# Performance work log

Hardware: AMD Instinct MI355X
Metric: run time of the kernel (lower is better)

The kernel has to match this reference:

```python
import jax, jax.numpy as jnp
import numpy as np

B, H, W, C = 16, 128, 128, 192
WS, SHIFT, HEADS = 8, 4, 6
N = WS * WS
HD = C // HEADS
SCALE = HD ** -0.5
EPS = 1e-5


def _rel_pos_index():
    coords = np.stack(np.meshgrid(np.arange(WS), np.arange(WS), indexing='ij')).reshape(2, -1)
    rel = (coords[:, :, None] - coords[:, None, :]).transpose(1, 2, 0)
    rel[..., 0] += WS - 1
    rel[..., 1] += WS - 1
    rel[..., 0] *= 2 * WS - 1
    return rel.sum(-1)  # [N, N] int


def _attn_mask():
    img = np.zeros((H, W), np.float32)
    sl = [(0, H - WS), (H - WS, H - SHIFT), (H - SHIFT, H)]
    cnt = 0
    for h0, h1 in sl:
        for w0, w1 in sl:
            img[h0:h1, w0:w1] = cnt
            cnt += 1
    mw = img.reshape(H // WS, WS, W // WS, WS).transpose(0, 2, 1, 3).reshape(-1, N)
    am = mw[:, None, :] - mw[:, :, None]
    return np.where(am != 0, np.float32(-100.0), np.float32(0.0))  # [nW, N, N]


REL_IDX = jnp.asarray(_rel_pos_index())
ATTN_MASK = jnp.asarray(_attn_mask())


def _ln(x, g, b):
    mu = x.mean(-1, keepdims=True)
    var = ((x - mu) ** 2).mean(-1, keepdims=True)
    return (x - mu) * jax.lax.rsqrt(var + EPS) * g + b


def setup_inputs() -> dict:
    key = jax.random.key(0)
    ks = jax.random.split(key, 12)
    d = {
        'x': jax.random.normal(ks[0], (B, H * W, C), jnp.float32),
        'norm1_g': jnp.ones((C,), jnp.float32),
        'norm1_b': jnp.zeros((C,), jnp.float32),
        'qkv_w': jax.random.normal(ks[1], (3 * C, C), jnp.float32) * 0.02,
        'qkv_b': jnp.zeros((3 * C,), jnp.float32),
        'proj_w': jax.random.normal(ks[2], (C, C), jnp.float32) * 0.02,
        'proj_b': jnp.zeros((C,), jnp.float32),
        'rpb_table': jax.random.normal(ks[3], ((2 * WS - 1) ** 2, HEADS), jnp.float32) * 0.02,
        'norm2_g': jnp.ones((C,), jnp.float32),
        'norm2_b': jnp.zeros((C,), jnp.float32),
        'fc1_w': jax.random.normal(ks[4], (4 * C, C), jnp.float32) * 0.02,
        'fc1_b': jnp.zeros((4 * C,), jnp.float32),
        'fc2_w': jax.random.normal(ks[5], (C, 4 * C), jnp.float32) * 0.02,
        'fc2_b': jnp.zeros((C,), jnp.float32),
    }
    return d


def reference(x, norm1_g, norm1_b, qkv_w, qkv_b, proj_w, proj_b, rpb_table,
              norm2_g, norm2_b, fc1_w, fc1_b, fc2_w, fc2_b):
    shortcut = x
    h = _ln(x, norm1_g, norm1_b).reshape(B, H, W, C)
    # cyclic shift (SW-MSA)
    h = jnp.roll(h, shift=(-SHIFT, -SHIFT), axis=(1, 2))
    # window partition -> [B*nW, N, C]
    h = h.reshape(B, H // WS, WS, W // WS, WS, C).transpose(0, 1, 3, 2, 4, 5)
    xw = h.reshape(-1, N, C)
    Bw = xw.shape[0]
    nW = (H // WS) * (W // WS)
    # qkv projection
    qkv = xw @ qkv_w.T + qkv_b  # [Bw, N, 3C]
    qkv = qkv.reshape(Bw, N, 3, HEADS, HD).transpose(2, 0, 3, 1, 4)
    q, k, v = qkv[0], qkv[1], qkv[2]  # [Bw, HEADS, N, HD]
    attn = jnp.einsum('bhnd,bhmd->bhnm', q * SCALE, k)
    # relative position bias gather: [N*N, HEADS] -> [HEADS, N, N]
    bias = rpb_table[REL_IDX.reshape(-1)].reshape(N, N, HEADS).transpose(2, 0, 1)
    attn = attn + bias[None]
    # shift mask add per-window
    attn = attn.reshape(B, nW, HEADS, N, N) + ATTN_MASK[None, :, None, :, :]
    attn = jax.nn.softmax(attn.reshape(Bw, HEADS, N, N), axis=-1)
    out = jnp.einsum('bhnm,bhmd->bhnd', attn, v)
    out = out.transpose(0, 2, 1, 3).reshape(Bw, N, C)
    out = out @ proj_w.T + proj_b
    # window reverse
    out = out.reshape(B, H // WS, W // WS, WS, WS, C).transpose(0, 1, 3, 2, 4, 5)
    out = out.reshape(B, H, W, C)
    out = jnp.roll(out, shift=(SHIFT, SHIFT), axis=(1, 2)).reshape(B, H * W, C)
    h = shortcut + out
    # MLP with residual
    m = _ln(h, norm2_g, norm2_b)
    m = jax.nn.gelu(m @ fc1_w.T + fc1_b, approximate=False)
    m = m @ fc2_w.T + fc2_b
    return h + m
```

## Files before the change

kernel.cpp:

```cpp
#include <hip/hip_runtime.h>
#include <hip/hip_bf16.h>

typedef __bf16 bf16;
typedef __bf16 bf16x8 __attribute__((ext_vector_type(8)));
typedef float f32x4 __attribute__((ext_vector_type(4)));

#define MFMA16(a, b, c) __builtin_amdgcn_mfma_f32_16x16x32_bf16(a, b, c, 0, 0, 0)

#define SCALE_Q 0.17677669529663687f

__global__ __launch_bounds__(256) void prep_kernel(
    const float* __restrict__ qkv_w, const float* __restrict__ proj_w,
    const float* __restrict__ fc1_w, const float* __restrict__ fc2_w,
    const float* __restrict__ rpb,
    bf16* __restrict__ wqkv, bf16* __restrict__ wproj,
    bf16* __restrict__ wfc1, bf16* __restrict__ wfc2,
    float* __restrict__ bias_full) {
  const int i = blockIdx.x * 256 + threadIdx.x;
  if (i < 110592) wqkv[i] = (bf16)qkv_w[i];
  if (i < 36864)  wproj[i] = (bf16)proj_w[i];
  if (i < 147456) { wfc1[i] = (bf16)fc1_w[i]; wfc2[i] = (bf16)fc2_w[i]; }
  if (i < 24576) {
    const int head = i >> 12;
    const int row = (i >> 6) & 63, col = i & 63;
    const int idx = ((row >> 3) - (col >> 3) + 7) * 15 + ((row & 7) - (col & 7) + 7);
    bias_full[i] = rpb[idx * 6 + head];
  }
}

__device__ __forceinline__ int region8(int tok, int wy, int wx) {
  const int gh = wy * 8 + (tok >> 3), gw = wx * 8 + (tok & 7);
  const int rs = (gh < 120) ? 0 : ((gh < 124) ? 1 : 2);
  const int cs = (gw < 120) ? 0 : ((gw < 124) ? 1 : 2);
  return rs * 3 + cs;
}

__global__ __launch_bounds__(384, 3) void swin_block_kernel(
    const float* __restrict__ x,
    const float* __restrict__ n1g, const float* __restrict__ n1b,
    const bf16* __restrict__ wqkv, const float* __restrict__ qkv_b,
    const bf16* __restrict__ wproj, const float* __restrict__ proj_b,
    const float* __restrict__ bias_full,
    const float* __restrict__ n2g, const float* __restrict__ n2b,
    const bf16* __restrict__ wfc1, const float* __restrict__ fc1_b,
    const bf16* __restrict__ wfc2, const float* __restrict__ fc2_b,
    float* __restrict__ out) {
  __shared__ __align__(16) char smem[80896];
  bf16*  a_s  = (bf16*)(smem);
  bf16*  q_s  = (bf16*)(smem);
  bf16*  k_s  = (bf16*)(smem + 24576);
  bf16*  vT_s = (bf16*)(smem + 49152);
  bf16*  ao_s = (bf16*)(smem);
  float* red_s = (float*)(smem + 25600);
  bf16*  m_s  = (bf16*)(smem + 29696);
  bf16*  g_s  = (bf16*)(smem + 55296);

  const int lane = threadIdx.x & 63, waveid = threadIdx.x >> 6;
  const int c = lane & 15, quad = lane >> 4;
  const int window = blockIdx.x;
  const int bi = window >> 8, w_in = window & 255;
  const int wy = w_in >> 4, wx = w_in & 15;
  const f32x4 fzero = {0.f, 0.f, 0.f, 0.f};

  auto p_ptr = [&](int head, int row, int colbyte) -> bf16* {
    int off = (row << 7) + colbyte;
    off ^= (row & 7) << 4;
    return (bf16*)(smem + (head << 13) + off);
  };

  for (int it = 0; it < 11; it++) {
    const int n = waveid * 11 + it;
    if (n < 64) {
      const int oh = (wy * 8 + (n >> 3) + 4) & 127;
      const int ow = (wx * 8 + (n & 7) + 4) & 127;
      const float* xr = x + (size_t)(bi * 16384 + oh * 128 + ow) * 192;
      float v0 = xr[lane], v1 = xr[lane + 64], v2 = xr[lane + 128];
      float s = v0 + v1 + v2;
      float s2 = v0 * v0 + v1 * v1 + v2 * v2;
#pragma unroll
      for (int off = 1; off < 64; off <<= 1) {
        s += __shfl_xor(s, off);
        s2 += __shfl_xor(s2, off);
      }
      const float mu = s * (1.f / 192.f);
      const float rinv = rsqrtf(s2 * (1.f / 192.f) - mu * mu + 1e-5f);
      a_s[n * 200 + lane]       = (bf16)((v0 - mu) * rinv * n1g[lane]       + n1b[lane]);
      a_s[n * 200 + lane + 64]  = (bf16)((v1 - mu) * rinv * n1g[lane + 64]  + n1b[lane + 64]);
      a_s[n * 200 + lane + 128] = (bf16)((v2 - mu) * rinv * n1g[lane + 128] + n1b[lane + 128]);
    }
  }
  __syncthreads();

  {
    f32x4 acc[4][6];
#pragma unroll
    for (int i = 0; i < 4; i++)
#pragma unroll
      for (int j = 0; j < 6; j++) acc[i][j] = fzero;
#pragma unroll
    for (int ks = 0; ks < 6; ks++) {
      bf16x8 a[4], w[6];
#pragma unroll
      for (int i = 0; i < 4; i++)
        a[i] = *(const bf16x8*)&a_s[(16 * i + c) * 200 + ks * 32 + quad * 8];
#pragma unroll
      for (int j = 0; j < 6; j++)
        w[j] = *(const bf16x8*)(wqkv +
            (size_t)(waveid * 96 + 16 * j + c) * 192 + ks * 32 + quad * 8);
#pragma unroll
      for (int i = 0; i < 4; i++)
#pragma unroll
        for (int j = 0; j < 6; j++) acc[i][j] = MFMA16(a[i], w[j], acc[i][j]);
    }
    __syncthreads();
    const int which = waveid >> 1;
#pragma unroll
    for (int j = 0; j < 6; j++) {
      const int col = waveid * 96 + 16 * j + c;
      const int sub = col - which * 192;
      const int head = sub >> 5, d = sub & 31;
      const float bias = qkv_b[col];
#pragma unroll
      for (int i = 0; i < 4; i++)
#pragma unroll
        for (int r = 0; r < 4; r++) {
          const int n = 16 * i + 4 * quad + r;
          const float val = acc[i][j][r] + bias;
          if (which == 0)      q_s[head * 2048 + n * 32 + d] = (bf16)(val * SCALE_Q);
          else if (which == 1) k_s[head * 2048 + n * 32 + d] = (bf16)val;
          else                 vT_s[head * 2048 + d * 64 + n] = (bf16)val;
        }
    }
  }
  __syncthreads();

  f32x4 o[4][2];
  {
    const int head = waveid;
    bf16x8 aq[4], bk[4];
#pragma unroll
    for (int i = 0; i < 4; i++)
      aq[i] = *(const bf16x8*)&q_s[head * 2048 + (16 * i + c) * 32 + quad * 8];
#pragma unroll
    for (int j = 0; j < 4; j++)
      bk[j] = *(const bf16x8*)&k_s[head * 2048 + (16 * j + c) * 32 + quad * 8];
    __syncthreads();

    f32x4 s[4][4];
#pragma unroll
    for (int i = 0; i < 4; i++)
#pragma unroll
      for (int j = 0; j < 4; j++) s[i][j] = fzero;
#pragma unroll
    for (int i = 0; i < 4; i++)
#pragma unroll
      for (int j = 0; j < 4; j++) s[i][j] = MFMA16(aq[i], bk[j], s[i][j]);

    const float* bfp = bias_full + head * 4096;
#pragma unroll
    for (int i = 0; i < 4; i++)
#pragma unroll
      for (int r = 0; r < 4; r++) {
        const int row = 16 * i + 4 * quad + r;
#pragma unroll
        for (int j = 0; j < 4; j++) s[i][j][r] += bfp[row * 64 + 16 * j + c];
      }

    if (wy == 15 || wx == 15) {
      int creg[4];
#pragma unroll
      for (int j = 0; j < 4; j++) creg[j] = region8(16 * j + c, wy, wx);
#pragma unroll
      for (int i = 0; i < 4; i++)
#pragma unroll
        for (int r = 0; r < 4; r++) {
          const int rreg = region8(16 * i + 4 * quad + r, wy, wx);
#pragma unroll
          for (int j = 0; j < 4; j++)
            if (rreg != creg[j]) s[i][j][r] -= 100.f;
        }
    }

#pragma unroll
    for (int i = 0; i < 4; i++)
#pragma unroll
      for (int r = 0; r < 4; r++) {
        float mx = fmaxf(fmaxf(s[i][0][r], s[i][1][r]), fmaxf(s[i][2][r], s[i][3][r]));
#pragma unroll
        for (int off = 1; off < 16; off <<= 1) mx = fmaxf(mx, __shfl_xor(mx, off));
        float sum = 0.f;
#pragma unroll
        for (int j = 0; j < 4; j++) {
          const float p = __expf(s[i][j][r] - mx);
          s[i][j][r] = p;
          sum += p;
        }
#pragma unroll
        for (int off = 1; off < 16; off <<= 1) sum += __shfl_xor(sum, off);
        const float inv = 1.f / sum;
        const int row = 16 * i + 4 * quad + r;
#pragma unroll
        for (int j = 0; j < 4; j++)
          *p_ptr(head, row, (16 * j + c) * 2) = (bf16)(s[i][j][r] * inv);
      }

#pragma unroll
    for (int i = 0; i < 4; i++)
#pragma unroll
      for (int tn = 0; tn < 2; tn++) o[i][tn] = fzero;
#pragma unroll
    for (int ks = 0; ks < 2; ks++) {
      bf16x8 ap[4], bv[2];
#pragma unroll
      for (int i = 0; i < 4; i++)
        ap[i] = *(const bf16x8*)p_ptr(head, 16 * i + c, ks * 64 + quad * 16);
#pragma unroll
      for (int tn = 0; tn < 2; tn++)
        bv[tn] = *(const bf16x8*)&vT_s[head * 2048 + (16 * tn + c) * 64 + ks * 32 + quad * 8];
#pragma unroll
      for (int i = 0; i < 4; i++)
#pragma unroll
        for (int tn = 0; tn < 2; tn++) o[i][tn] = MFMA16(ap[i], bv[tn], o[i][tn]);
    }
  }
  __syncthreads();

#pragma unroll
  for (int i = 0; i < 4; i++)
#pragma unroll
    for (int tn = 0; tn < 2; tn++)
#pragma unroll
      for (int r = 0; r < 4; r++)
        ao_s[(16 * i + 4 * quad + r) * 200 + waveid * 32 + 16 * tn + c] = (bf16)o[i][tn][r];
  __syncthreads();

  float hreg[4][2][4];
  {
    f32x4 acc[4][2];
#pragma unroll
    for (int i = 0; i < 4; i++)
#pragma unroll
      for (int j = 0; j < 2; j++) acc[i][j] = fzero;
#pragma unroll
    for (int ks = 0; ks < 6; ks++) {
      bf16x8 a[4], w[2];
#pragma unroll
      for (int i = 0; i < 4; i++)
        a[i] = *(const bf16x8*)&ao_s[(16 * i + c) * 200 + ks * 32 + quad * 8];
#pragma unroll
      for (int j = 0; j < 2; j++)
        w[j] = *(const bf16x8*)(wproj +
            (size_t)(waveid * 32 + 16 * j + c) * 192 + ks * 32 + quad * 8);
#pragma unroll
      for (int i = 0; i < 4; i++)
#pragma unroll
        for (int j = 0; j < 2; j++) acc[i][j] = MFMA16(a[i], w[j], acc[i][j]);
    }
#pragma unroll
    for (int i = 0; i < 4; i++)
#pragma unroll
      for (int r = 0; r < 4; r++) {
        const int n = 16 * i + 4 * quad + r;
        const int oh = (wy * 8 + (n >> 3) + 4) & 127;
        const int ow = (wx * 8 + (n & 7) + 4) & 127;
        const float* xr = x + (size_t)(bi * 16384 + oh * 128 + ow) * 192;
#pragma unroll
        for (int j = 0; j < 2; j++) {
          const int col = waveid * 32 + 16 * j + c;
          hreg[i][j][r] = acc[i][j][r] + proj_b[col] + xr[col];
        }
      }
  }

#pragma unroll
  for (int i = 0; i < 4; i++)
#pragma unroll
    for (int r = 0; r < 4; r++) {
      float s1 = hreg[i][0][r] + hreg[i][1][r];
      float s2 = hreg[i][0][r] * hreg[i][0][r] + hreg[i][1][r] * hreg[i][1][r];
#pragma unroll
      for (int off = 1; off < 16; off <<= 1) {
        s1 += __shfl_xor(s1, off);
        s2 += __shfl_xor(s2, off);
      }
      if (c == 0) {
        const int n = 16 * i + 4 * quad + r;
        red_s[n * 16 + waveid] = s1;
        red_s[n * 16 + 8 + waveid] = s2;
      }
    }
  __syncthreads();
  {
    const int col0 = waveid * 32 + c, col1 = col0 + 16;
    const float g0 = n2g[col0], b0 = n2b[col0];
    const float g1 = n2g[col1], b1 = n2b[col1];
#pragma unroll
    for (int i = 0; i < 4; i++)
#pragma unroll
      for (int r = 0; r < 4; r++) {
        const int n = 16 * i + 4 * quad + r;
        const f32x4 lo = *(const f32x4*)&red_s[n * 16 + 0];
        const f32x4 hi = *(const f32x4*)&red_s[n * 16 + 4];
        const f32x4 qlo = *(const f32x4*)&red_s[n * 16 + 8];
        const f32x4 qhi = *(const f32x4*)&red_s[n * 16 + 12];
        const float s1 = lo[0] + lo[1] + lo[2] + lo[3] + hi[0] + hi[1];
        const float s2 = qlo[0] + qlo[1] + qlo[2] + qlo[3] + qhi[0] + qhi[1];
        const float mu = s1 * (1.f / 192.f);
        const float rinv = rsqrtf(s2 * (1.f / 192.f) - mu * mu + 1e-5f);
        m_s[n * 200 + col0] = (bf16)((hreg[i][0][r] - mu) * rinv * g0 + b0);
        m_s[n * 200 + col1] = (bf16)((hreg[i][1][r] - mu) * rinv * g1 + b1);
      }
  }
  __syncthreads();

  f32x4 oacc[4][2];
#pragma unroll
  for (int i = 0; i < 4; i++)
#pragma unroll
    for (int j = 0; j < 2; j++) oacc[i][j] = fzero;

  for (int chunk = 0; chunk < 4; chunk++) {
    f32x4 gacc[4][2];
#pragma unroll
    for (int i = 0; i < 4; i++)
#pragma unroll
      for (int j = 0; j < 2; j++) gacc[i][j] = fzero;
#pragma unroll
    for (int ks = 0; ks < 6; ks++) {
      bf16x8 a[4], w[2];
#pragma unroll
      for (int i = 0; i < 4; i++)
        a[i] = *(const bf16x8*)&m_s[(16 * i + c) * 200 + ks * 32 + quad * 8];
#pragma unroll
      for (int j = 0; j < 2; j++)
        w[j] = *(const bf16x8*)(wfc1 +
            (size_t)(chunk * 192 + waveid * 32 + 16 * j + c) * 192 + ks * 32 + quad * 8);
#pragma unroll
      for (int i = 0; i < 4; i++)
#pragma unroll
        for (int j = 0; j < 2; j++) gacc[i][j] = MFMA16(a[i], w[j], gacc[i][j]);
    }
#pragma unroll
    for (int i = 0; i < 4; i++)
#pragma unroll
      for (int j = 0; j < 2; j++) {
        const int lcol = waveid * 32 + 16 * j + c;
        const float fb = fc1_b[chunk * 192 + lcol];
#pragma unroll
        for (int r = 0; r < 4; r++) {
          float val = gacc[i][j][r] + fb;
          val = 0.5f * val * (1.f + erff(val * 0.70710678118654752f));
          g_s[(16 * i + 4 * quad + r) * 200 + lcol] = (bf16)val;
        }
      }
    __syncthreads();
#pragma unroll
    for (int ks = 0; ks < 6; ks++) {
      bf16x8 a[4], w[2];
#pragma unroll
      for (int i = 0; i < 4; i++)
        a[i] = *(const bf16x8*)&g_s[(16 * i + c) * 200 + ks * 32 + quad * 8];
#pragma unroll
      for (int j = 0; j < 2; j++)
        w[j] = *(const bf16x8*)(wfc2 +
            (size_t)(waveid * 32 + 16 * j + c) * 768 + chunk * 192 + ks * 32 + quad * 8);
#pragma unroll
      for (int i = 0; i < 4; i++)
#pragma unroll
        for (int j = 0; j < 2; j++) oacc[i][j] = MFMA16(a[i], w[j], oacc[i][j]);
    }
    __syncthreads();
  }

#pragma unroll
  for (int i = 0; i < 4; i++)
#pragma unroll
    for (int r = 0; r < 4; r++) {
      const int n = 16 * i + 4 * quad + r;
      const int oh = (wy * 8 + (n >> 3) + 4) & 127;
      const int ow = (wx * 8 + (n & 7) + 4) & 127;
      float* orow = out + (size_t)(bi * 16384 + oh * 128 + ow) * 192;
#pragma unroll
      for (int j = 0; j < 2; j++) {
        const int col = waveid * 32 + 16 * j + c;
        orow[col] = oacc[i][j][r] + fc2_b[col] + hreg[i][j][r];
      }
    }
}

extern "C" void kernel_launch(void* const* d_in, const int* in_sizes, int n_in,
                              void* d_out, int out_size, void* d_ws, size_t ws_size,
                              hipStream_t stream) {
  const float* x      = (const float*)d_in[0];
  const float* n1g    = (const float*)d_in[1];
  const float* n1b    = (const float*)d_in[2];
  const float* qkv_w  = (const float*)d_in[3];
  const float* qkv_b  = (const float*)d_in[4];
  const float* proj_w = (const float*)d_in[5];
  const float* proj_b = (const float*)d_in[6];
  const float* rpb    = (const float*)d_in[7];
  const float* n2g    = (const float*)d_in[8];
  const float* n2b    = (const float*)d_in[9];
  const float* fc1_w  = (const float*)d_in[10];
  const float* fc1_b  = (const float*)d_in[11];
  const float* fc2_w  = (const float*)d_in[12];
  const float* fc2_b  = (const float*)d_in[13];

  char* ws = (char*)d_ws;
  float* biasf = (float*)(ws);
  bf16*  wqkv  = (bf16*)(ws + 98304);
  bf16*  wproj = (bf16*)(ws + 98304 + 221184);
  bf16*  wfc1  = (bf16*)(ws + 98304 + 221184 + 73728);
  bf16*  wfc2  = (bf16*)(ws + 98304 + 221184 + 73728 + 294912);

  prep_kernel<<<576, 256, 0, stream>>>(qkv_w, proj_w, fc1_w, fc2_w, rpb,
                                       wqkv, wproj, wfc1, wfc2, biasf);
  swin_block_kernel<<<4096, 384, 0, stream>>>(
      x, n1g, n1b, wqkv, qkv_b, wproj, proj_b, biasf,
      n2g, n2b, wfc1, fc1_b, wfc2, fc2_b, (float*)d_out);
}
```

Baseline: 1.419 ms.

## Spill residual to output buffer, pad V transpose, relax launch bounds

Writes the attention residual h to the output buffer right away and reads it back from global memory in the final epilogue, rather than keeping 32 floats live in registers across the MLP. Stores the transposed V with a padded stride of 72 and packed 4-wide bf16 writes to cut LDS bank conflicts, and reorganises shared memory so the m/g/reduction buffers alias earlier regions. Launch bounds minimum blocks drops from 3 to 1, giving the compiler more registers at the possible cost of occupancy. The extra global round-trip of h adds memory traffic.

Measured after the change: 1.292 ms. 1.1x faster.

```diff
diff --git a/kernel.cpp b/kernel.cpp
--- a/kernel.cpp
+++ b/kernel.cpp
@@ -2,6 +2,7 @@
 #include <hip/hip_bf16.h>
 
 typedef __bf16 bf16;
+typedef __bf16 bf16x4 __attribute__((ext_vector_type(4)));
 typedef __bf16 bf16x8 __attribute__((ext_vector_type(8)));
 typedef float f32x4 __attribute__((ext_vector_type(4)));
 
@@ -35,7 +36,7 @@
   return rs * 3 + cs;
 }
 
-__global__ __launch_bounds__(384, 3) void swin_block_kernel(
+__global__ __launch_bounds__(384, 1) void swin_block_kernel(
     const float* __restrict__ x,
     const float* __restrict__ n1g, const float* __restrict__ n1b,
     const bf16* __restrict__ wqkv, const float* __restrict__ qkv_b,
@@ -45,15 +46,15 @@
     const bf16* __restrict__ wfc1, const float* __restrict__ fc1_b,
     const bf16* __restrict__ wfc2, const float* __restrict__ fc2_b,
     float* __restrict__ out) {
-  __shared__ __align__(16) char smem[80896];
+  __shared__ __align__(16) char smem[76800];
   bf16*  a_s  = (bf16*)(smem);
   bf16*  q_s  = (bf16*)(smem);
   bf16*  k_s  = (bf16*)(smem + 24576);
   bf16*  vT_s = (bf16*)(smem + 49152);
   bf16*  ao_s = (bf16*)(smem);
-  float* red_s = (float*)(smem + 25600);
-  bf16*  m_s  = (bf16*)(smem + 29696);
-  bf16*  g_s  = (bf16*)(smem + 55296);
+  bf16*  m_s  = (bf16*)(smem);
+  bf16*  g_s  = (bf16*)(smem + 25600);
+  float* red_s = (float*)(smem + 51200);
 
   const int lane = threadIdx.x & 63, waveid = threadIdx.x >> 6;
   const int c = lane & 15, quad = lane >> 4;
@@ -114,22 +115,38 @@
     }
     __syncthreads();
     const int which = waveid >> 1;
-#pragma unroll
-    for (int j = 0; j < 6; j++) {
-      const int col = waveid * 96 + 16 * j + c;
-      const int sub = col - which * 192;
-      const int head = sub >> 5, d = sub & 31;
-      const float bias = qkv_b[col];
-#pragma unroll
-      for (int i = 0; i < 4; i++)
-#pragma unroll
-        for (int r = 0; r < 4; r++) {
-          const int n = 16 * i + 4 * quad + r;
-          const float val = acc[i][j][r] + bias;
-          if (which == 0)      q_s[head * 2048 + n * 32 + d] = (bf16)(val * SCALE_Q);
-          else if (which == 1) k_s[head * 2048 + n * 32 + d] = (bf16)val;
-          else                 vT_s[head * 2048 + d * 64 + n] = (bf16)val;
+    if (which == 2) {
+#pragma unroll
+      for (int j = 0; j < 6; j++) {
+        const int col = waveid * 96 + 16 * j + c;
+        const int sub = col - 384;
+        const int head = sub >> 5, d = sub & 31;
+        const float bias = qkv_b[col];
+#pragma unroll
+        for (int i = 0; i < 4; i++) {
+          bf16x4 pk;
+#pragma unroll
+          for (int r = 0; r < 4; r++) pk[r] = (bf16)(acc[i][j][r] + bias);
+          *(bf16x4*)&vT_s[head * 2304 + d * 72 + 16 * i + 4 * quad] = pk;
         }
+      }
+    } else {
+#pragma unroll
+      for (int j = 0; j < 6; j++) {
+        const int col = waveid * 96 + 16 * j + c;
+        const int sub = col - which * 192;
+        const int head = sub >> 5, d = sub & 31;
+        const float bias = qkv_b[col];
+#pragma unroll
+        for (int i = 0; i < 4; i++)
+#pragma unroll
+          for (int r = 0; r < 4; r++) {
+            const int n = 16 * i + 4 * quad + r;
+            const float val = acc[i][j][r] + bias;
+            if (which == 0) q_s[head * 2048 + n * 32 + d] = (bf16)(val * SCALE_Q);
+            else            k_s[head * 2048 + n * 32 + d] = (bf16)val;
+          }
+      }
     }
   }
   __syncthreads();
@@ -216,7 +233,7 @@
         ap[i] = *(const bf16x8*)p_ptr(head, 16 * i + c, ks * 64 + quad * 16);
 #pragma unroll
       for (int tn = 0; tn < 2; tn++)
-        bv[tn] = *(const bf16x8*)&vT_s[head * 2048 + (16 * tn + c) * 64 + ks * 32 + quad * 8];
+        bv[tn] = *(const bf16x8*)&vT_s[head * 2304 + (16 * tn + c) * 72 + ks * 32 + quad * 8];
 #pragma unroll
       for (int i = 0; i < 4; i++)
 #pragma unroll
@@ -234,7 +251,7 @@
         ao_s[(16 * i + 4 * quad + r) * 200 + waveid * 32 + 16 * tn + c] = (bf16)o[i][tn][r];
   __syncthreads();
 
-  float hreg[4][2][4];
+  float hv[4][2][4];
   {
     f32x4 acc[4][2];
 #pragma unroll
@@ -263,11 +280,15 @@
         const int n = 16 * i + 4 * quad + r;
         const int oh = (wy * 8 + (n >> 3) + 4) & 127;
         const int ow = (wx * 8 + (n & 7) + 4) & 127;
-        const float* xr = x + (size_t)(bi * 16384 + oh * 128 + ow) * 192;
+        const size_t base = (size_t)(bi * 16384 + oh * 128 + ow) * 192;
+        const float* xr = x + base;
+        float* orow = out + base;
 #pragma unroll
         for (int j = 0; j < 2; j++) {
           const int col = waveid * 32 + 16 * j + c;
-          hreg[i][j][r] = acc[i][j][r] + proj_b[col] + xr[col];
+          const float h = acc[i][j][r] + proj_b[col] + xr[col];
+          hv[i][j][r] = h;
+          orow[col] = h;
         }
       }
   }
@@ -276,8 +297,8 @@
   for (int i = 0; i < 4; i++)
 #pragma unroll
     for (int r = 0; r < 4; r++) {
-      float s1 = hreg[i][0][r] + hreg[i][1][r];
-      float s2 = hreg[i][0][r] * hreg[i][0][r] + hreg[i][1][r] * hreg[i][1][r];
+      float s1 = hv[i][0][r] + hv[i][1][r];
+      float s2 = hv[i][0][r] * hv[i][0][r] + hv[i][1][r] * hv[i][1][r];
 #pragma unroll
       for (int off = 1; off < 16; off <<= 1) {
         s1 += __shfl_xor(s1, off);
@@ -290,6 +311,7 @@
       }
     }
   __syncthreads();
+
   {
     const int col0 = waveid * 32 + c, col1 = col0 + 16;
     const float g0 = n2g[col0], b0 = n2b[col0];
@@ -307,8 +329,8 @@
         const float s2 = qlo[0] + qlo[1] + qlo[2] + qlo[3] + qhi[0] + qhi[1];
         const float mu = s1 * (1.f / 192.f);
         const float rinv = rsqrtf(s2 * (1.f / 192.f) - mu * mu + 1e-5f);
-        m_s[n * 200 + col0] = (bf16)((hreg[i][0][r] - mu) * rinv * g0 + b0);
-        m_s[n * 200 + col1] = (bf16)((hreg[i][1][r] - mu) * rinv * g1 + b1);
+        m_s[n * 200 + col0] = (bf16)((hv[i][0][r] - mu) * rinv * g0 + b0);
+        m_s[n * 200 + col1] = (bf16)((hv[i][1][r] - mu) * rinv * g1 + b1);
       }
   }
   __syncthreads();
@@ -383,7 +405,8 @@
 #pragma unroll
       for (int j = 0; j < 2; j++) {
         const int col = waveid * 32 + 16 * j + c;
-        orow[col] = oacc[i][j][r] + fc2_b[col] + hreg[i][j][r];
+        const float h = orow[col];
+        orow[col] = oacc[i][j][r] + fc2_b[col] + h;
       }
     }
 }
```
